# Kernel tuning notes

Measured on AMD Instinct MI355X. Metric: run time of the kernel, lower is better.

Reference implementation:

```python
import jax, jax.numpy as jnp
import numpy as np

EPS = 1e-5

def _ln(x, g, b):
    m = jnp.mean(x, axis=-1, keepdims=True)
    v = jnp.mean((x - m) ** 2, axis=-1, keepdims=True)
    return (x - m) * jax.lax.rsqrt(v + EPS) * g + b

def setup_inputs() -> dict:
    key = jax.random.key(0)
    B, T, V, D = 32, 512, 16, 128
    ks = jax.random.split(key, 22)
    rn = lambda k, shp, sc: jax.random.normal(k, shp, jnp.float32) * sc
    inp = {
        "x": rn(ks[0], (B, T, V), 1.0),
        # per-variable GRN params (stacked over the V variables)
        "W1": rn(ks[1], (V, D), 1.0),          # fc1: Linear(1, D) weight per var
        "b1": rn(ks[2], (V, D), 0.02),
        "W2": rn(ks[3], (V, D, D), 1.0 / np.sqrt(D)),   # fc2: Linear(D, D)
        "b2": rn(ks[4], (V, D), 0.02),
        "Wg": rn(ks[5], (V, D, D), 1.0 / np.sqrt(D)),   # gate: Linear(D, D)
        "bg": rn(ks[6], (V, D), 0.02),
        "Ws": rn(ks[7], (V, D), 1.0),          # skip: Linear(1, D)
        "bs": rn(ks[8], (V, D), 0.02),
        "gamma": jnp.ones((V, D), jnp.float32),
        "beta": jnp.zeros((V, D), jnp.float32),
        # softmax GRN params: d_in = V*D, d_hidden = D, d_out = V
        "sW1": rn(ks[9], (D, V * D), 1.0 / np.sqrt(V * D)),
        "sb1": rn(ks[10], (D,), 0.02),
        "sW2": rn(ks[11], (V, D), 1.0 / np.sqrt(D)),
        "sb2": rn(ks[12], (V,), 0.02),
        "sWg": rn(ks[13], (V, D), 1.0 / np.sqrt(D)),
        "sbg": rn(ks[14], (V,), 0.02),
        "sWs": rn(ks[15], (V, V * D), 1.0 / np.sqrt(V * D)),
        "sbs": rn(ks[16], (V,), 0.02),
        "sgamma": jnp.ones((V,), jnp.float32),
        "sbeta": jnp.zeros((V,), jnp.float32),
    }
    return inp

def reference(x, W1, b1, W2, b2, Wg, bg, Ws, bs, gamma, beta,
              sW1, sb1, sW2, sb2, sWg, sbg, sWs, sbs, sgamma, sbeta):
    V, D = W1.shape
    lead = x.shape[:-1]
    xf = x.reshape(-1, V)                                  # (N, V)
    # ---- all per-variable GRNs batched over the var dim ----
    h = jax.nn.elu(xf[..., None] * W1 + b1)                # (N, V, D)
    h2 = jnp.einsum('nvd,vod->nvo', h, W2) + b2            # (N, V, D)
    g = jax.nn.sigmoid(jnp.einsum('nvd,vod->nvo', h, Wg) + bg)
    skip = xf[..., None] * Ws + bs                         # (N, V, D)
    stacked = _ln(g * h2 + (1.0 - g) * skip, gamma, beta)  # (N, V, D)
    # ---- softmax GRN over flattened embeddings ----
    flat = stacked.reshape(-1, V * D)                      # (N, V*D)
    hs = jax.nn.elu(flat @ sW1.T + sb1)                    # (N, D)
    h2s = hs @ sW2.T + sb2                                 # (N, V)
    gs = jax.nn.sigmoid(hs @ sWg.T + sbg)
    sks = flat @ sWs.T + sbs
    weights = jax.nn.softmax(_ln(gs * h2s + (1.0 - gs) * sks, sgamma, sbeta), axis=-1)
    processed = jnp.einsum('nvd,nv->nd', stacked, weights) # (N, D)
    return processed.reshape(*lead, D), weights.reshape(*lead, V)
```

## Files before the change

kernel.cpp:

```cpp
#include <hip/hip_runtime.h>
#include <hip/hip_bf16.h>
#include <math.h>

#define NVAR 16
#define ND 128
#define NVD 2048
#define NROWS 16384
#define RTA 256
#define NRB 64

typedef short s16x8 __attribute__((ext_vector_type(8)));
typedef short s16x4 __attribute__((ext_vector_type(4)));
typedef float f32x4 __attribute__((ext_vector_type(4)));
typedef unsigned short u16;

#define MFMA(a,b,c) __builtin_amdgcn_mfma_f32_16x16x32_bf16((a),(b),(c),0,0,0)

#define OFF_W2  0
#define OFF_WG  262144
#define OFF_SW1 524288
#define OFF_SWS 786432
#define OFF_SW2 819200
#define OFF_SWG 821248
#define WS_ELEMS 823296
#define OFF_STK 823296
#define STK_ELEMS ((size_t)NROWS*NVD)
#define WS_NEEDED_BYTES (((size_t)WS_ELEMS + STK_ELEMS)*2)

__device__ __forceinline__ unsigned f2bf(float f){
    union { float f; unsigned u; } c; c.f = f;
    unsigned u = c.u;
    u += 0x7fffu + ((u >> 16) & 1u);
    return u >> 16;
}
__device__ __forceinline__ float bf2f(unsigned bits){
    union { unsigned u; float f; } c; c.u = bits << 16;
    return c.f;
}
__device__ __forceinline__ float eluf(float x){ return x > 0.f ? x : __expf(x) - 1.f; }
__device__ __forceinline__ float sigm(float x){
    return __builtin_amdgcn_rcpf(1.f + __expf(-x));
}

__device__ __forceinline__ int offBig(int r, int c){
    return r*2048 + ((((c>>3) ^ (r&7))<<3) | (c&7));
}
__device__ __forceinline__ int offHs(int r, int c){
    return r*128 + ((((c>>3) ^ (r&7))<<3) | (c&7));
}

__global__ void prep_kernel(const float* __restrict__ W2, const float* __restrict__ Wg,
                            const float* __restrict__ sW1, const float* __restrict__ sWs,
                            const float* __restrict__ sW2, const float* __restrict__ sWg,
                            u16* __restrict__ ws){
    int i = blockIdx.x*256 + threadIdx.x;
    if (i >= WS_ELEMS) return;
    float v;
    if      (i < OFF_WG)  v = W2[i];
    else if (i < OFF_SW1) v = Wg[i-OFF_WG];
    else if (i < OFF_SWS) v = sW1[i-OFF_SW1];
    else if (i < OFF_SW2) v = sWs[i-OFF_SWS];
    else if (i < OFF_SWG) v = sW2[i-OFF_SW2];
    else                  v = sWg[i-OFF_SWG];
    ws[i] = (u16)f2bf(v);
}

__global__ __launch_bounds__(512, 2)
void vsn_varA(const float* __restrict__ x,
              const float* __restrict__ W1, const float* __restrict__ b1,
              const float* __restrict__ b2, const float* __restrict__ bg,
              const float* __restrict__ Wsk, const float* __restrict__ bsk,
              const float* __restrict__ gamma, const float* __restrict__ beta,
              u16* __restrict__ ws)
{
    __shared__ u16 lw2[128*128];
    __shared__ u16 lwg[128*128];
    __shared__ u16 hbuf[8*16*128];
    __shared__ u16 obuf[8*16*128];
    __shared__ float lp[8*128];
    __shared__ float lxv[RTA];

    const int t = threadIdx.x, w = t>>6, l = t&63;
    const int hr = l>>4, c16 = l&15;
    const int v = blockIdx.y;
    const int row0 = blockIdx.x*RTA;

    #pragma unroll
    for (int i=0;i<8;++i){
        int cid = i*512 + t;
        int mat = cid>>11, within = cid&2047;
        int r = within>>4, c8 = within&15;
        const u16* src = ws + (mat? OFF_WG:OFF_W2) + v*16384 + r*128 + c8*8;
        s16x8 val = *reinterpret_cast<const s16x8*>(src);
        u16* dst = (mat? lwg:lw2) + r*128 + ((c8 ^ (r&7))<<3);
        *reinterpret_cast<s16x8*>(dst) = val;
    }
    if (t < 128){
        lp[t]     = W1[v*ND+t];    lp[128+t] = b1[v*ND+t];
        lp[256+t] = b2[v*ND+t];    lp[384+t] = bg[v*ND+t];
        lp[512+t] = Wsk[v*ND+t];   lp[640+t] = bsk[v*ND+t];
        lp[768+t] = gamma[v*ND+t]; lp[896+t] = beta[v*ND+t];
    }
    if (t < RTA) lxv[t] = x[(size_t)(row0+t)*NVAR + v];
    __syncthreads();

    u16* hb = hbuf + w*2048;
    u16* ob = obuf + w*2048;
    #pragma unroll 1
    for (int pass=0; pass<2; ++pass){
        const int g = w + pass*8;
        const int lrow0 = g*16;

        {
            int r = l>>2, cb = (l&3)*32;
            float xv = lxv[lrow0 + r];
            #pragma unroll
            for (int cc=0; cc<4; ++cc){
                s16x8 o;
                #pragma unroll
                for (int j=0;j<8;++j){
                    int c = cb + cc*8 + j;
                    o[j] = (short)f2bf(eluf(xv*lp[c] + lp[128+c]));
                }
                int chunk = (((cb>>3) + cc) ^ (r&7));
                *reinterpret_cast<s16x8*>(hb + r*128 + chunk*8) = o;
            }
        }
        s16x8 B[4];
        #pragma unroll
        for (int ks=0;ks<4;++ks){
            int chunk = (ks*4 + hr) ^ (c16&7);
            B[ks] = *reinterpret_cast<const s16x8*>(hb + c16*128 + chunk*8);
        }
        const float xnv = lxv[lrow0 + c16];
        float y[8][4];
        #pragma unroll
        for (int ct=0; ct<8; ++ct){
            f32x4 a2 = {0.f,0.f,0.f,0.f}, ag = {0.f,0.f,0.f,0.f};
            const int wr = ct*16 + c16;
            #pragma unroll
            for (int ks=0;ks<4;++ks){
                int chunk = (ks*4 + hr) ^ (wr&7);
                s16x8 A2 = *reinterpret_cast<const s16x8*>(lw2 + wr*128 + chunk*8);
                a2 = MFMA(A2, B[ks], a2);
            }
            #pragma unroll
            for (int ks=0;ks<4;++ks){
                int chunk = (ks*4 + hr) ^ (wr&7);
                s16x8 Ag = *reinterpret_cast<const s16x8*>(lwg + wr*128 + chunk*8);
                ag = MFMA(Ag, B[ks], ag);
            }
            const int obb = ct*16 + hr*4;
            float4 b2v = *reinterpret_cast<const float4*>(&lp[256+obb]);
            float4 bgv = *reinterpret_cast<const float4*>(&lp[384+obb]);
            float4 wsv = *reinterpret_cast<const float4*>(&lp[512+obb]);
            float4 bsv = *reinterpret_cast<const float4*>(&lp[640+obb]);
            #pragma unroll
            for (int j=0;j<4;++j){
                float h2 = a2[j] + reinterpret_cast<const float*>(&b2v)[j];
                float gg = sigm(ag[j] + reinterpret_cast<const float*>(&bgv)[j]);
                float sk = xnv*reinterpret_cast<const float*>(&wsv)[j]
                           + reinterpret_cast<const float*>(&bsv)[j];
                y[ct][j] = gg*h2 + (1.f-gg)*sk;
            }
        }
        float s = 0.f, q = 0.f;
        #pragma unroll
        for (int ct=0;ct<8;++ct)
            #pragma unroll
            for (int j=0;j<4;++j){ float yy = y[ct][j]; s += yy; q += yy*yy; }
        s += __shfl_xor(s, 16); s += __shfl_xor(s, 32);
        q += __shfl_xor(q, 16); q += __shfl_xor(q, 32);
        float mean = s*(1.f/ND);
        float inv  = rsqrtf(q*(1.f/ND) - mean*mean + 1e-5f);

        #pragma unroll
        for (int ct=0;ct<8;++ct){
            const int obb = ct*16 + hr*4;
            float4 gm = *reinterpret_cast<const float4*>(&lp[768+obb]);
            float4 bt = *reinterpret_cast<const float4*>(&lp[896+obb]);
            s16x4 o;
            #pragma unroll
            for (int j=0;j<4;++j){
                float z = (y[ct][j]-mean)*inv*reinterpret_cast<const float*>(&gm)[j]
                          + reinterpret_cast<const float*>(&bt)[j];
                o[j] = (short)f2bf(z);
            }
            int chunk = ((obb>>3) ^ (c16&7));
            *reinterpret_cast<s16x4*>(ob + c16*128 + chunk*8 + (hr&1)*4) = o;
        }
        __syncthreads();

        {
            u16* stkbase = ws + OFF_STK + (size_t)(row0 + pass*128 + w*16)*NVD + v*ND;
            #pragma unroll
            for (int i=0;i<4;++i){
                int c = i*64 + l;
                int lr = c>>4, cc = c&15;
                int sch = cc ^ (lr&7);
                s16x8 val = *reinterpret_cast<const s16x8*>(ob + lr*128 + sch*8);
                *reinterpret_cast<s16x8*>(stkbase + (size_t)lr*NVD + cc*8) = val;
            }
        }
        __syncthreads();
    }
}

__global__ __launch_bounds__(512, 4)
void vsn_softB(const u16* __restrict__ ws,
               const float* __restrict__ sb1, const float* __restrict__ sb2,
               const float* __restrict__ sbg, const float* __restrict__ sbs,
               const float* __restrict__ sgamma, const float* __restrict__ sbeta,
               float* __restrict__ out_proc, float* __restrict__ out_w)
{
    __shared__ u16   abuf[64*256];
    __shared__ u16   hsb[64*128];
    __shared__ float pps_[2*64*16];
    __shared__ float pph[64*16];
    __shared__ float ppg[64*16];
    __shared__ float sksf[64*16];
    __shared__ float wgtb[64*16];

    float* pps = pps_;

    const int t = threadIdx.x, w = t>>6, l = t&63;
    const int hr = l>>4, c16 = l&15;
    const int row0 = blockIdx.x * NRB;
    const int orow = w*16 + c16;
    const int rgs = w & 3;
    const int khf = w >> 2;

    const u16* stk  = ws + OFF_STK;
    const u16* sW1b = ws + OFF_SW1;
    const u16* sWsb = ws + OFF_SWS;

    f32x4 accHs[4] = {{0,0,0,0},{0,0,0,0},{0,0,0,0},{0,0,0,0}};
    f32x4 accSk = {0,0,0,0};

    #pragma unroll 1
    for (int kt=0; kt<8; ++kt){
        #pragma unroll
        for (int i=0;i<4;++i){
            int cid = i*512 + t;
            int r = cid>>5, c8 = cid&31;
            s16x8 val = *reinterpret_cast<const s16x8*>(
                stk + (size_t)(row0+r)*NVD + kt*256 + c8*8);
            *reinterpret_cast<s16x8*>(abuf + r*256 + ((c8 ^ (r&7))<<3)) = val;
        }
        __syncthreads();
        #pragma unroll
        for (int ks=0; ks<8; ++ks){
            s16x8 bf = *reinterpret_cast<const s16x8*>(
                sW1b + (size_t)orow*NVD + kt*256 + ks*32 + hr*8);
            #pragma unroll
            for (int rg=0; rg<4; ++rg){
                int rr = rg*16 + c16;
                int chunk = (ks*4 + hr) ^ (rr&7);
                s16x8 af = *reinterpret_cast<const s16x8*>(abuf + rr*256 + chunk*8);
                accHs[rg] = MFMA(af, bf, accHs[rg]);
            }
        }
        #pragma unroll
        for (int kk=0; kk<4; ++kk){
            int ks = khf*4 + kk;
            s16x8 bf = *reinterpret_cast<const s16x8*>(
                sWsb + (size_t)c16*NVD + kt*256 + ks*32 + hr*8);
            int rr = rgs*16 + c16;
            int chunk = (ks*4 + hr) ^ (rr&7);
            s16x8 af = *reinterpret_cast<const s16x8*>(abuf + rr*256 + chunk*8);
            accSk = MFMA(af, bf, accSk);
        }
        __syncthreads();
    }

    {
        float bb = sb1[orow];
        #pragma unroll
        for (int rg=0; rg<4; ++rg){
            #pragma unroll
            for (int j=0;j<4;++j){
                int r = rg*16 + hr*4 + j;
                hsb[offHs(r, orow)] = (u16)f2bf(eluf(accHs[rg][j] + bb));
            }
        }
        #pragma unroll
        for (int j=0;j<4;++j)
            pps[khf*1024 + (rgs*16 + hr*4 + j)*16 + c16] = accSk[j];
    }
    __syncthreads();

    #pragma unroll
    for (int i=0;i<2;++i){
        int idx = i*512 + t;
        sksf[idx] = pps[idx] + pps[1024+idx] + sbs[idx&15];
    }
    {
        const u16* Bsrc = (w < 4) ? (ws + OFF_SW2) : (ws + OFF_SWG);
        int rg = w & 3;
        f32x4 acc = {0,0,0,0};
        #pragma unroll
        for (int ks=0; ks<4; ++ks){
            int rr = rg*16 + c16;
            int chunk = (ks*4 + hr) ^ (rr&7);
            s16x8 af = *reinterpret_cast<const s16x8*>(hsb + rr*128 + chunk*8);
            s16x8 bf = *reinterpret_cast<const s16x8*>(Bsrc + c16*ND + ks*32 + hr*8);
            acc = MFMA(af, bf, acc);
        }
        float* dst = (w < 4) ? pph : ppg;
        #pragma unroll
        for (int j=0;j<4;++j)
            dst[(rg*16 + hr*4 + j)*16 + c16] = acc[j];
    }
    __syncthreads();

    #pragma unroll
    for (int it=0; it<2; ++it){
        int r = it*32 + (t>>4), vv = t & 15;
        float h2s = pph[r*16+vv] + sb2[vv];
        float gs  = sigm(ppg[r*16+vv] + sbg[vv]);
        float yv  = gs*h2s + (1.f-gs)*sksf[r*16+vv];
        float ssum = yv, qsum = yv*yv;
        #pragma unroll
        for (int m=1;m<16;m<<=1){ ssum += __shfl_xor(ssum,m,16); qsum += __shfl_xor(qsum,m,16); }
        float mean = ssum*(1.f/NVAR);
        float var  = qsum*(1.f/NVAR) - mean*mean;
        float z = (yv-mean)*rsqrtf(var+1e-5f)*sgamma[vv] + sbeta[vv];
        float mx = z;
        #pragma unroll
        for (int m=1;m<16;m<<=1) mx = fmaxf(mx, __shfl_xor(mx,m,16));
        float e = __expf(z-mx);
        float es = e;
        #pragma unroll
        for (int m=1;m<16;m<<=1) es += __shfl_xor(es,m,16);
        float wgt = e * __builtin_amdgcn_rcpf(es);
        wgtb[r*16+vv] = wgt;
        out_w[(size_t)(row0+r)*NVAR + vv] = wgt;
    }
    __syncthreads();

    #pragma unroll
    for (int it=0; it<2; ++it){
        int idx = it*512 + t;
        int r = idx>>4, d8 = idx&15;
        float acc[8] = {0,0,0,0,0,0,0,0};
        const u16* sp = stk + (size_t)(row0+r)*NVD + d8*8;
        #pragma unroll
        for (int v=0; v<NVAR; ++v){
            float wv = wgtb[r*16 + v];
            s16x8 sv = *reinterpret_cast<const s16x8*>(sp + v*ND);
            #pragma unroll
            for (int k=0;k<8;++k) acc[k] += bf2f((u16)sv[k]) * wv;
        }
        float* op = out_proc + (size_t)(row0+r)*ND + d8*8;
        #pragma unroll
        for (int k=0;k<8;++k) op[k] = acc[k];
    }
}

__global__ __launch_bounds__(512, 4)
void vsn_fused(const float* __restrict__ x,
               const float* __restrict__ W1, const float* __restrict__ b1,
               const float* __restrict__ b2, const float* __restrict__ bg,
               const float* __restrict__ Wsk, const float* __restrict__ bsk,
               const float* __restrict__ gamma, const float* __restrict__ beta,
               const float* __restrict__ sb1, const float* __restrict__ sb2,
               const float* __restrict__ sbg, const float* __restrict__ sbs,
               const float* __restrict__ sgamma, const float* __restrict__ sbeta,
               const u16* __restrict__ ws,
               float* __restrict__ out_proc, float* __restrict__ out_w)
{
    __shared__ u16   big[16*2048];
    __shared__ u16   hsb[16*128];
    __shared__ float pp[8*256];
    __shared__ float psumbuf[256];
    __shared__ float sksbuf[256];
    __shared__ float sx[256];

    float* psum  = psumbuf;
    float* psum2 = psumbuf + 128;

    const int t   = threadIdx.x;
    const int w   = t >> 6;
    const int l   = t & 63;
    const int hr  = l >> 4;
    const int c16 = l & 15;
    const int row0 = blockIdx.x * 16;
    const int orow = w*16 + c16;

    if (t < 256) sx[t] = x[row0*NVAR + t];
    __syncthreads();

    const u16* W2b = ws + OFF_W2;
    const u16* Wgb = ws + OFF_WG;

    for (int v = 0; v < NVAR; ++v){
        #pragma unroll
        for (int i = 0; i < 4; ++i){
            int idx = i*512 + t;
            int r = idx >> 7, d = idx & 127;
            float hv = eluf(sx[r*NVAR+v]*W1[v*ND+d] + b1[v*ND+d]);
            big[offBig(r, v*ND+d)] = (u16)f2bf(hv);
        }
        __syncthreads();

        s16x8 A[4];
        #pragma unroll
        for (int ks = 0; ks < 4; ++ks)
            A[ks] = *reinterpret_cast<const s16x8*>(&big[offBig(c16, v*ND + ks*32 + hr*8)]);
        const s16x8* B2p = reinterpret_cast<const s16x8*>(W2b + v*ND*ND + orow*ND + hr*8);
        const s16x8* Bgp = reinterpret_cast<const s16x8*>(Wgb + v*ND*ND + orow*ND + hr*8);
        f32x4 acc2 = {0.f,0.f,0.f,0.f}, accg = {0.f,0.f,0.f,0.f};
        #pragma unroll
        for (int ks = 0; ks < 4; ++ks) acc2 = MFMA(A[ks], B2p[ks*4], acc2);
        #pragma unroll
        for (int ks = 0; ks < 4; ++ks) accg = MFMA(A[ks], Bgp[ks*4], accg);

        const float b2v = b2[v*ND+orow], bgv = bg[v*ND+orow];
        const float wsv = Wsk[v*ND+orow], bsv = bsk[v*ND+orow];
        float y[4];
        #pragma unroll
        for (int j = 0; j < 4; ++j){
            int r = hr*4 + j;
            float h2 = acc2[j] + b2v;
            float g  = sigm(accg[j] + bgv);
            float sk = sx[r*NVAR+v]*wsv + bsv;
            y[j] = g*h2 + (1.f-g)*sk;
        }
        float s[4], q[4];
        #pragma unroll
        for (int j=0;j<4;++j){ s[j]=y[j]; q[j]=y[j]*y[j]; }
        #pragma unroll
        for (int m=1; m<16; m<<=1){
            #pragma unroll
            for (int j=0;j<4;++j){
                s[j] += __shfl_xor(s[j], m, 16);
                q[j] += __shfl_xor(q[j], m, 16);
            }
        }
        if (c16 == 0){
            #pragma unroll
            for (int j=0;j<4;++j){
                psum [(hr*4+j)*8 + w] = s[j];
                psum2[(hr*4+j)*8 + w] = q[j];
            }
        }
        __syncthreads();

        if (t < 16){
            float ss=0.f, qq=0.f;
            #pragma unroll
            for (int ww=0; ww<8; ++ww){ ss += psum[t*8+ww]; qq += psum2[t*8+ww]; }
            float mean = ss*(1.f/ND);
            float var  = qq*(1.f/ND) - mean*mean;
            sksbuf[t]      = mean;
            sksbuf[16 + t] = rsqrtf(var + 1e-5f);
        }
        __syncthreads();

        const float gm = gamma[v*ND+orow], bt = beta[v*ND+orow];
        #pragma unroll
        for (int j=0;j<4;++j){
            int r = hr*4 + j;
            float z = (y[j]-sksbuf[r])*sksbuf[16+r]*gm + bt;
            big[offBig(r, v*ND+orow)] = (u16)f2bf(z);
        }
    }
    __syncthreads();

    const u16* sW1b = ws + OFF_SW1;
    {
        f32x4 acc0 = {0,0,0,0}, acc1 = {0,0,0,0};
        const s16x8* Bp = reinterpret_cast<const s16x8*>(sW1b + orow*NVD + hr*8);
        #pragma unroll 8
        for (int ks = 0; ks < 64; ks += 2){
            s16x8 A0 = *reinterpret_cast<const s16x8*>(&big[offBig(c16, ks*32 + hr*8)]);
            s16x8 A1 = *reinterpret_cast<const s16x8*>(&big[offBig(c16, (ks+1)*32 + hr*8)]);
            acc0 = MFMA(A0, Bp[ks*4],     acc0);
            acc1 = MFMA(A1, Bp[(ks+1)*4], acc1);
        }
        float bb = sb1[orow];
        #pragma unroll
        for (int j=0;j<4;++j){
            int r = hr*4 + j;
            hsb[offHs(r, orow)] = (u16)f2bf(eluf(acc0[j] + acc1[j] + bb));
        }
    }
    const u16* sWsb = ws + OFF_SWS;
    {
        f32x4 acc = {0,0,0,0};
        const s16x8* Bp = reinterpret_cast<const s16x8*>(sWsb + c16*NVD + hr*8);
        #pragma unroll
        for (int kk = 0; kk < 8; ++kk){
            int ks = w*8 + kk;
            s16x8 Af = *reinterpret_cast<const s16x8*>(&big[offBig(c16, ks*32 + hr*8)]);
            acc = MFMA(Af, Bp[ks*4], acc);
        }
        #pragma unroll
        for (int j=0;j<4;++j)
            pp[w*256 + (hr*4+j)*16 + c16] = acc[j];
    }
    __syncthreads();

    if (t < 256){
        float a = sbs[t & 15];
        #pragma unroll
        for (int ww=0; ww<8; ++ww) a += pp[ww*256 + t];
        sksbuf[t] = a;
    }
    __syncthreads();

    {
        const u16* Bsrc = (w < 4) ? (ws + OFF_SW2) : (ws + OFF_SWG);
        const int m = w & 3;
        s16x8 Af = *reinterpret_cast<const s16x8*>(&hsb[offHs(c16, m*32 + hr*8)]);
        s16x8 Bf = *reinterpret_cast<const s16x8*>(Bsrc + c16*ND + m*32 + hr*8);
        f32x4 z4 = {0,0,0,0};
        f32x4 acc = MFMA(Af, Bf, z4);
        #pragma unroll
        for (int j=0;j<4;++j)
            pp[w*256 + (hr*4+j)*16 + c16] = acc[j];
    }
    __syncthreads();

    if (t < 256){
        int r = t >> 4, vv = t & 15;
        float h2s = sb2[vv], gp = sbg[vv];
        #pragma unroll
        for (int j=0;j<4;++j){ h2s += pp[j*256 + t]; gp += pp[(4+j)*256 + t]; }
        float gs = sigm(gp);
        float yv = gs*h2s + (1.f-gs)*sksbuf[t];
        float ssum = yv, qsum = yv*yv;
        #pragma unroll
        for (int m=1;m<16;m<<=1){ ssum += __shfl_xor(ssum,m,16); qsum += __shfl_xor(qsum,m,16); }
        float mean = ssum*(1.f/NVAR);
        float var  = qsum*(1.f/NVAR) - mean*mean;
        float z = (yv-mean)*rsqrtf(var+1e-5f)*sgamma[vv] + sbeta[vv];
        float mx = z;
        #pragma unroll
        for (int m=1;m<16;m<<=1) mx = fmaxf(mx, __shfl_xor(mx,m,16));
        float e = __expf(z-mx);
        float es = e;
        #pragma unroll
        for (int m=1;m<16;m<<=1) es += __shfl_xor(es,m,16);
        float wgt = e/es;
        psumbuf[t] = wgt;
        out_w[(row0+r)*NVAR + vv] = wgt;
    }
    __syncthreads();

    if (t < 256){
        int r = t >> 4, d8 = (t & 15)*8;
        float acc[8] = {0,0,0,0,0,0,0,0};
        #pragma unroll
        for (int v=0; v<NVAR; ++v){
            float wv = psumbuf[r*NVAR + v];
            s16x8 sv = *reinterpret_cast<const s16x8*>(&big[offBig(r, v*ND + d8)]);
            #pragma unroll
            for (int k=0;k<8;++k) acc[k] += bf2f((u16)sv[k]) * wv;
        }
        float* op = &out_proc[(row0+r)*ND + d8];
        #pragma unroll
        for (int k=0;k<8;++k) op[k] = acc[k];
    }
}

extern "C" void kernel_launch(void* const* d_in, const int* in_sizes, int n_in,
                              void* d_out, int out_size, void* d_ws, size_t ws_size,
                              hipStream_t stream) {
    (void)in_sizes; (void)n_in; (void)out_size;
    const float* x     = (const float*)d_in[0];
    const float* W1    = (const float*)d_in[1];
    const float* b1    = (const float*)d_in[2];
    const float* W2    = (const float*)d_in[3];
    const float* b2    = (const float*)d_in[4];
    const float* Wg    = (const float*)d_in[5];
    const float* bg    = (const float*)d_in[6];
    const float* Wsk   = (const float*)d_in[7];
    const float* bsk   = (const float*)d_in[8];
    const float* gamma = (const float*)d_in[9];
    const float* beta  = (const float*)d_in[10];
    const float* sW1   = (const float*)d_in[11];
    const float* sb1   = (const float*)d_in[12];
    const float* sW2   = (const float*)d_in[13];
    const float* sb2   = (const float*)d_in[14];
    const float* sWg   = (const float*)d_in[15];
    const float* sbg   = (const float*)d_in[16];
    const float* sWs   = (const float*)d_in[17];
    const float* sbs   = (const float*)d_in[18];
    const float* sgam  = (const float*)d_in[19];
    const float* sbet  = (const float*)d_in[20];

    u16* ws = (u16*)d_ws;
    float* out_proc = (float*)d_out;
    float* out_w    = out_proc + (size_t)NROWS * ND;

    prep_kernel<<<(WS_ELEMS + 255)/256, 256, 0, stream>>>(W2, Wg, sW1, sWs, sW2, sWg, ws);

    if (ws_size >= WS_NEEDED_BYTES) {
        vsn_varA<<<dim3(NROWS/RTA, NVAR), 512, 0, stream>>>(
            x, W1, b1, b2, bg, Wsk, bsk, gamma, beta, ws);
        vsn_softB<<<NROWS/NRB, 512, 0, stream>>>(
            ws, sb1, sb2, sbg, sbs, sgam, sbet, out_proc, out_w);
    } else {
        vsn_fused<<<NROWS/16, 512, 0, stream>>>(
            x, W1, b1, b2, bg, Wsk, bsk, gamma, beta,
            sb1, sb2, sbg, sbs, sgam, sbet, ws, out_proc, out_w);
    }
}
```

Before: 126.9 us.

## Store stacked activations in MFMA-fragment layout and compute ELU operands in registers

The variable GRN kernel now builds the ELU B-operand fragments directly in registers instead of staging them through shared memory. It also writes the layer-normed outputs straight to global memory in a per-variable, per-16-row-group fragment layout, with no LDS staging or block barriers. The consumer kernel's tile loads, A-fragment reads and final weighted sum are rewritten to match this layout, using a new swizzle and two half-vector LDS reads per fragment. This removes shared-memory traffic and synchronisation in the producer, at the cost of more complex addressing and split LDS reads in the consumer.

```diff
diff --git a/kernel.cpp b/kernel.cpp
--- a/kernel.cpp
+++ b/kernel.cpp
@@ -26,6 +26,7 @@
 #define OFF_STK 823296
 #define STK_ELEMS ((size_t)NROWS*NVD)
 #define WS_NEEDED_BYTES (((size_t)WS_ELEMS + STK_ELEMS)*2)
+#define SV_ELEMS ((size_t)(NROWS/16)*2048)
 
 __device__ __forceinline__ unsigned f2bf(float f){
     union { float f; unsigned u; } c; c.f = f;
@@ -42,11 +43,11 @@
     return __builtin_amdgcn_rcpf(1.f + __expf(-x));
 }
 
+__device__ __forceinline__ int offHs(int r, int c){
+    return r*128 + ((((c>>3) ^ (r&7))<<3) | (c&7));
+}
 __device__ __forceinline__ int offBig(int r, int c){
     return r*2048 + ((((c>>3) ^ (r&7))<<3) | (c&7));
-}
-__device__ __forceinline__ int offHs(int r, int c){
-    return r*128 + ((((c>>3) ^ (r&7))<<3) | (c&7));
 }
 
 __global__ void prep_kernel(const float* __restrict__ W2, const float* __restrict__ Wg,
@@ -75,8 +76,6 @@
 {
     __shared__ u16 lw2[128*128];
     __shared__ u16 lwg[128*128];
-    __shared__ u16 hbuf[8*16*128];
-    __shared__ u16 obuf[8*16*128];
     __shared__ float lp[8*128];
     __shared__ float lxv[RTA];
 
@@ -104,35 +103,23 @@
     if (t < RTA) lxv[t] = x[(size_t)(row0+t)*NVAR + v];
     __syncthreads();
 
-    u16* hb = hbuf + w*2048;
-    u16* ob = obuf + w*2048;
     #pragma unroll 1
     for (int pass=0; pass<2; ++pass){
-        const int g = w + pass*8;
-        const int lrow0 = g*16;
-
-        {
-            int r = l>>2, cb = (l&3)*32;
-            float xv = lxv[lrow0 + r];
-            #pragma unroll
-            for (int cc=0; cc<4; ++cc){
-                s16x8 o;
-                #pragma unroll
-                for (int j=0;j<8;++j){
-                    int c = cb + cc*8 + j;
-                    o[j] = (short)f2bf(eluf(xv*lp[c] + lp[128+c]));
-                }
-                int chunk = (((cb>>3) + cc) ^ (r&7));
-                *reinterpret_cast<s16x8*>(hb + r*128 + chunk*8) = o;
-            }
-        }
+        const int lrow0 = (w + pass*8)*16;
+        const float xv = lxv[lrow0 + c16];
+
         s16x8 B[4];
         #pragma unroll
         for (int ks=0;ks<4;++ks){
-            int chunk = (ks*4 + hr) ^ (c16&7);
-            B[ks] = *reinterpret_cast<const s16x8*>(hb + c16*128 + chunk*8);
-        }
-        const float xnv = lxv[lrow0 + c16];
+            s16x8 o;
+            #pragma unroll
+            for (int j=0;j<8;++j){
+                int c = ks*32 + hr*8 + j;
+                o[j] = (short)f2bf(eluf(xv*lp[c] + lp[128+c]));
+            }
+            B[ks] = o;
+        }
+
         float y[8][4];
         #pragma unroll
         for (int ct=0; ct<8; ++ct){
@@ -159,7 +146,7 @@
             for (int j=0;j<4;++j){
                 float h2 = a2[j] + reinterpret_cast<const float*>(&b2v)[j];
                 float gg = sigm(ag[j] + reinterpret_cast<const float*>(&bgv)[j]);
-                float sk = xnv*reinterpret_cast<const float*>(&wsv)[j]
+                float sk = xv*reinterpret_cast<const float*>(&wsv)[j]
                            + reinterpret_cast<const float*>(&bsv)[j];
                 y[ct][j] = gg*h2 + (1.f-gg)*sk;
             }
@@ -174,36 +161,40 @@
         float mean = s*(1.f/ND);
         float inv  = rsqrtf(q*(1.f/ND) - mean*mean + 1e-5f);
 
-        #pragma unroll
-        for (int ct=0;ct<8;++ct){
-            const int obb = ct*16 + hr*4;
-            float4 gm = *reinterpret_cast<const float4*>(&lp[768+obb]);
-            float4 bt = *reinterpret_cast<const float4*>(&lp[896+obb]);
-            s16x4 o;
-            #pragma unroll
-            for (int j=0;j<4;++j){
-                float z = (y[ct][j]-mean)*inv*reinterpret_cast<const float*>(&gm)[j]
-                          + reinterpret_cast<const float*>(&bt)[j];
-                o[j] = (short)f2bf(z);
-            }
-            int chunk = ((obb>>3) ^ (c16&7));
-            *reinterpret_cast<s16x4*>(ob + c16*128 + chunk*8 + (hr&1)*4) = o;
-        }
-        __syncthreads();
-
-        {
-            u16* stkbase = ws + OFF_STK + (size_t)(row0 + pass*128 + w*16)*NVD + v*ND;
-            #pragma unroll
-            for (int i=0;i<4;++i){
-                int c = i*64 + l;
-                int lr = c>>4, cc = c&15;
-                int sch = cc ^ (lr&7);
-                s16x8 val = *reinterpret_cast<const s16x8*>(ob + lr*128 + sch*8);
-                *reinterpret_cast<s16x8*>(stkbase + (size_t)lr*NVD + cc*8) = val;
-            }
-        }
-        __syncthreads();
-    }
+        const int grp = blockIdx.x*16 + w + pass*8;
+        u16* stkb = ws + OFF_STK + (size_t)v*SV_ELEMS + (size_t)grp*2048;
+        #pragma unroll
+        for (int ctp=0; ctp<4; ++ctp){
+            s16x8 o;
+            #pragma unroll
+            for (int hh=0; hh<2; ++hh){
+                int ct = ctp*2 + hh;
+                const int obb = ct*16 + hr*4;
+                float4 gm = *reinterpret_cast<const float4*>(&lp[768+obb]);
+                float4 bt = *reinterpret_cast<const float4*>(&lp[896+obb]);
+                #pragma unroll
+                for (int j=0;j<4;++j){
+                    float z = (y[ct][j]-mean)*inv*reinterpret_cast<const float*>(&gm)[j]
+                              + reinterpret_cast<const float*>(&bt)[j];
+                    o[hh*4+j] = (short)f2bf(z);
+                }
+            }
+            *reinterpret_cast<s16x8*>(stkb + ctp*512 + c16*32 + hr*8) = o;
+        }
+    }
+}
+
+__device__ __forceinline__ s16x8 ldA(const u16* abuf, int vrel, int rg, int ctp, int n, int hr){
+    int base = (((vrel*4 + rg)*4 + ctp)*16 + n)*32;
+    int fn = (n>>1)&3;
+    int u0 = (hr&1)*2;
+    int half = (hr>>1)*4;
+    s16x4 lo = *reinterpret_cast<const s16x4*>(abuf + base + (((u0  )^fn)<<3) + half);
+    s16x4 hi = *reinterpret_cast<const s16x4*>(abuf + base + (((u0+1)^fn)<<3) + half);
+    s16x8 r;
+    r[0]=lo[0]; r[1]=lo[1]; r[2]=lo[2]; r[3]=lo[3];
+    r[4]=hi[0]; r[5]=hi[1]; r[6]=hi[2]; r[7]=hi[3];
+    return r;
 }
 
 __global__ __launch_bounds__(512, 4)
@@ -213,7 +204,7 @@
                const float* __restrict__ sgamma, const float* __restrict__ sbeta,
                float* __restrict__ out_proc, float* __restrict__ out_w)
 {
-    __shared__ u16   abuf[64*256];
+    __shared__ u16   abuf[16384];
     __shared__ u16   hsb[64*128];
     __shared__ float pps_[2*64*16];
     __shared__ float pph[64*16];
@@ -226,6 +217,7 @@
     const int t = threadIdx.x, w = t>>6, l = t&63;
     const int hr = l>>4, c16 = l&15;
     const int row0 = blockIdx.x * NRB;
+    const int grp0 = row0 >> 4;
     const int orow = w*16 + c16;
     const int rgs = w & 3;
     const int khf = w >> 2;
@@ -242,10 +234,14 @@
         #pragma unroll
         for (int i=0;i<4;++i){
             int cid = i*512 + t;
-            int r = cid>>5, c8 = cid&31;
-            s16x8 val = *reinterpret_cast<const s16x8*>(
-                stk + (size_t)(row0+r)*NVD + kt*256 + c8*8);
-            *reinterpret_cast<s16x8*>(abuf + r*256 + ((c8 ^ (r&7))<<3)) = val;
+            int vv  = kt*2 + (cid>>10);
+            int rg  = (cid>>8)&3;
+            int n   = (cid>>2)&15;
+            int u   = cid&3;
+            const u16* src = stk + (size_t)vv*SV_ELEMS + (size_t)(grp0+rg)*2048
+                           + ((cid>>2)&63)*32 + u*8;
+            s16x8 val = *reinterpret_cast<const s16x8*>(src);
+            *reinterpret_cast<s16x8*>(abuf + (cid>>2)*32 + ((u ^ ((n>>1)&3))<<3)) = val;
         }
         __syncthreads();
         #pragma unroll
@@ -254,9 +250,7 @@
                 sW1b + (size_t)orow*NVD + kt*256 + ks*32 + hr*8);
             #pragma unroll
             for (int rg=0; rg<4; ++rg){
-                int rr = rg*16 + c16;
-                int chunk = (ks*4 + hr) ^ (rr&7);
-                s16x8 af = *reinterpret_cast<const s16x8*>(abuf + rr*256 + chunk*8);
+                s16x8 af = ldA(abuf, ks>>2, rg, ks&3, c16, hr);
                 accHs[rg] = MFMA(af, bf, accHs[rg]);
             }
         }
@@ -265,9 +259,7 @@
             int ks = khf*4 + kk;
             s16x8 bf = *reinterpret_cast<const s16x8*>(
                 sWsb + (size_t)c16*NVD + kt*256 + ks*32 + hr*8);
-            int rr = rgs*16 + c16;
-            int chunk = (ks*4 + hr) ^ (rr&7);
-            s16x8 af = *reinterpret_cast<const s16x8*>(abuf + rr*256 + chunk*8);
+            s16x8 af = ldA(abuf, ks>>2, rgs, ks&3, c16, hr);
             accSk = MFMA(af, bf, accSk);
         }
         __syncthreads();
@@ -341,19 +333,24 @@
     #pragma unroll
     for (int it=0; it<2; ++it){
         int idx = it*512 + t;
-        int r = idx>>4, d8 = idx&15;
+        int r = idx>>4, cu = idx&15;
+        int ctp = cu>>2, u = cu&3;
+        int grp = (row0+r)>>4, n = r&15;
         float acc[8] = {0,0,0,0,0,0,0,0};
-        const u16* sp = stk + (size_t)(row0+r)*NVD + d8*8;
         #pragma unroll
         for (int v=0; v<NVAR; ++v){
             float wv = wgtb[r*16 + v];
-            s16x8 sv = *reinterpret_cast<const s16x8*>(sp + v*ND);
+            const u16* sp = stk + (size_t)v*SV_ELEMS + (size_t)grp*2048
+                          + (ctp*16+n)*32 + u*8;
+            s16x8 sv = *reinterpret_cast<const s16x8*>(sp);
             #pragma unroll
             for (int k=0;k<8;++k) acc[k] += bf2f((u16)sv[k]) * wv;
         }
-        float* op = out_proc + (size_t)(row0+r)*ND + d8*8;
-        #pragma unroll
-        for (int k=0;k<8;++k) op[k] = acc[k];
+        float* op = out_proc + (size_t)(row0+r)*ND + ctp*32 + u*4;
+        float4 lo = { acc[0], acc[1], acc[2], acc[3] };
+        float4 hi = { acc[4], acc[5], acc[6], acc[7] };
+        *reinterpret_cast<float4*>(op)      = lo;
+        *reinterpret_cast<float4*>(op + 16) = hi;
     }
 }
 
```

After: 457.3 us. 3.61x slower.
